# Optimization experiments

Hardware: AMD Instinct MI355X
Metric: run time of the kernel (lower is better)

The kernel has to match this reference:

```python
import jax, jax.numpy as jnp
import numpy as np

B, Cin, H, W = 8, 128, 64, 64
Cout, K, S, P = 128, 3, 1, 1
KK = K * K


def _conv(x, w, b=None):
    y = jax.lax.conv_general_dilated(
        x, w, window_strides=(S, S), padding=[(P, P), (P, P)],
        dimension_numbers=("NCHW", "OIHW", "NCHW"))
    if b is not None:
        y = y + b[None, :, None, None]
    return y


def setup_inputs() -> dict:
    key = jax.random.key(0)
    ks = jax.random.split(key, 6)
    x = jax.random.normal(ks[0], (B, Cin, H, W), jnp.float32)
    # offset/modulator convs are zero-init in the module; use small random
    # values so learned-offset sampling path is actually exercised.
    w_off = jax.random.normal(ks[1], (2 * KK, Cin, K, K), jnp.float32) * 0.01
    b_off = jax.random.normal(ks[2], (2 * KK,), jnp.float32) * 0.1
    w_mod = jax.random.normal(ks[3], (KK, Cin, K, K), jnp.float32) * 0.01
    b_mod = jax.random.normal(ks[4], (KK,), jnp.float32) * 0.1
    w_reg = jax.random.normal(ks[5], (Cout, Cin, K, K), jnp.float32) * (1.0 / np.sqrt(Cin * KK))
    return {"x": x, "w_off": w_off, "b_off": b_off,
            "w_mod": w_mod, "b_mod": b_mod, "w_reg": w_reg}


def _deform_conv2d(x, offset, mask, w_reg):
    # offset: [B, 2*KK, Hout, Wout] with (dy, dx) interleaved per tap (torchvision layout)
    Hout, Wout = offset.shape[2], offset.shape[3]
    off = offset.reshape(B, KK, 2, Hout, Wout)
    dy = off[:, :, 0].transpose(0, 2, 3, 1)  # [B,Hout,Wout,KK]
    dx = off[:, :, 1].transpose(0, 2, 3, 1)
    kh = (jnp.arange(KK) // K).astype(jnp.float32)
    kw = (jnp.arange(KK) % K).astype(jnp.float32)
    ho = jnp.arange(Hout, dtype=jnp.float32) * S - P
    wo = jnp.arange(Wout, dtype=jnp.float32) * S - P
    py = ho[None, :, None, None] + kh[None, None, None, :] + dy  # [B,Hout,Wout,KK]
    px = wo[None, None, :, None] + kw[None, None, None, :] + dx
    y0f = jnp.floor(py); x0f = jnp.floor(px)
    wy = (py - y0f)[..., None]; wx = (px - x0f)[..., None]
    y0 = y0f.astype(jnp.int32); x0 = x0f.astype(jnp.int32)
    x_bhwc = x.transpose(0, 2, 3, 1)  # [B,H,W,Cin]
    bidx = jnp.arange(B).reshape(B, 1, 1, 1)

    def gather(yi, xi):
        valid = ((yi >= 0) & (yi < H) & (xi >= 0) & (xi < W)).astype(x.dtype)
        v = x_bhwc[bidx, jnp.clip(yi, 0, H - 1), jnp.clip(xi, 0, W - 1)]
        return v * valid[..., None]  # [B,Hout,Wout,KK,Cin], zero outside

    v00 = gather(y0, x0)
    v01 = gather(y0, x0 + 1)
    v10 = gather(y0 + 1, x0)
    v11 = gather(y0 + 1, x0 + 1)
    val = (v00 * (1 - wy) * (1 - wx) + v01 * (1 - wy) * wx
           + v10 * wy * (1 - wx) + v11 * wy * wx)
    # modulated deformable conv v2: mask [B,KK,Hout,Wout]
    val = val * mask.transpose(0, 2, 3, 1)[..., None]
    # weighted accumulation over taps and input channels -> NCHW output
    return jnp.einsum("bhwkc,ock->bohw", val, w_reg.reshape(Cout, Cin, KK))


def reference(x, w_off, b_off, w_mod, b_mod, w_reg):
    offset = _conv(x, w_off, b_off)
    mask = 2.0 * jax.nn.sigmoid(_conv(x, w_mod, b_mod))
    return _deform_conv2d(x, offset, mask, w_reg)
```

## Files before the change

kernel.cpp:

```cpp
#include <hip/hip_runtime.h>
#include <hip/hip_bf16.h>
#include <math.h>

#define H 64
#define W 64
#define CIN 128
#define COUT 128
#define BATCH 8
#define NPIX (H*W)
#define PXT 32
#define AP  136
#define RP  36
#define VSZ (PXT*AP)

typedef __attribute__((ext_vector_type(8))) short bf16x8;
typedef __attribute__((ext_vector_type(2))) float f32x2;
typedef __attribute__((ext_vector_type(4))) float f32x4;
typedef __attribute__((ext_vector_type(16))) float f32x16;

static __device__ inline short f2bf(float f) {
  union { float f; unsigned u; } v; v.f = f;
  unsigned r = v.u + 0x7FFF + ((v.u >> 16) & 1);
  return (short)(r >> 16);
}
static __device__ inline f32x2 bfpair(unsigned u) {
  union { unsigned u; float f; } lo, hi;
  lo.u = u << 16; hi.u = u & 0xffff0000u;
  f32x2 r; r.x = lo.f; r.y = hi.f; return r;
}

__global__ __launch_bounds__(256) void k_prep(const float* __restrict__ x,
    short* __restrict__ xbh,
    const float* __restrict__ w_off, const float* __restrict__ w_mod,
    short* __restrict__ wOMs, const float* __restrict__ w_reg,
    short* __restrict__ wAs) {
  __shared__ float tile[32][65];
  int blk = blockIdx.x;
  int t = threadIdx.x;
  if (blk < 2048) {
    int cg = blk & 3, y = (blk >> 2) & 63, b = blk >> 8;
#pragma unroll
    for (int j = 0; j < 2; ++j) {
      int f = t + j * 256;
      int ci = f >> 4, xi4 = f & 15;
      float4 v = *(const float4*)&x[(((b * CIN + cg * 32 + ci) * H + y) * W) + xi4 * 4];
      *(float4*)&tile[ci][xi4 * 4] = v;
    }
    __syncthreads();
#pragma unroll
    for (int i = 0; i < 2; ++i) {
      int idx = t + i * 256;
      int xi = idx >> 3, cig = idx & 7;
      float f0 = tile[cig * 4 + 0][xi];
      float f1 = tile[cig * 4 + 1][xi];
      float f2 = tile[cig * 4 + 2][xi];
      float f3 = tile[cig * 4 + 3][xi];
      __hip_bfloat162 h01 = __float22bfloat162_rn(make_float2(f0, f1));
      __hip_bfloat162 h23 = __float22bfloat162_rn(make_float2(f2, f3));
      uint2 pk;
      pk.x = *(unsigned*)&h01; pk.y = *(unsigned*)&h23;
      *(uint2*)&xbh[((b * H + y) * W + xi) * CIN + cg * 32 + cig * 4] = pk;
    }
  } else if (blk < 2048 + 144) {
    int e = (blk - 2048) * 256 + t;
    int tap = e >> 12, oc = (e >> 7) & 31, c = e & 127;
    float v = 0.f;
    if (oc < 18)      v = w_off[(oc * 128 + c) * 9 + tap];
    else if (oc < 27) v = w_mod[((oc - 18) * 128 + c) * 9 + tap];
    int kstep = c >> 4, g = (c >> 3) & 1, j = c & 7;
    int lane = g * 32 + oc;
    int o = ((tap * 8 + kstep) * 64 + lane) * 8 + j;
    wOMs[o] = f2bf(v);
  } else {
    int e = (blk - 2192) * 256 + t;
    int tap = e >> 14, oc = (e >> 7) & 127, c = e & 127;
    int kstep = c >> 4, g = (c >> 3) & 1, j = c & 7;
    int ms = oc >> 5, m = oc & 31;
    int lane = g * 32 + m;
    int o = (((tap * 8 + kstep) * 4 + ms) * 64 + lane) * 8 + j;
    wAs[o] = f2bf(w_reg[(oc * 128 + c) * 9 + tap]);
  }
}

__global__ __launch_bounds__(512, 8) void k_deform(const short* __restrict__ xbh,
    const short* __restrict__ wOMs, const float* __restrict__ b_off,
    const float* __restrict__ b_mod, const short* __restrict__ wAs,
    float* __restrict__ out) {
  __shared__ __align__(16) char smem_u[31104];
  __shared__ __align__(16) float  pw[PXT * 9 * 4];
  __shared__ __align__(16) ushort pa4[PXT * 9 * 4];
  float* red  = (float*)smem_u;
  short* vs   = (short*)smem_u;
  float* redE = (float*)smem_u;

  int blk = blockIdx.x;
  int b = blk & 7, tile = blk >> 3;
  int pix0 = tile * PXT;
  int t = threadIdx.x;
  int lane = t & 63;
  int wv = t >> 6;
  int n32 = lane & 31, g = lane >> 5;

  const short* xbB = xbh + (size_t)b * NPIX * CIN;

  {
    f32x16 accO = {};
    int p0 = wv * 9;
    int tapA = p0 >> 3, tapB = (p0 + 8) >> 3;
    int gp = pix0 + n32;
    int yb = gp >> 6, xb = gp & 63;
    int yA = yb + tapA / 3 - 1, xA = xb + tapA % 3 - 1;
    int yB = yb + tapB / 3 - 1, xB = xb + tapB % 3 - 1;
    int okA = ((unsigned)yA < H) && ((unsigned)xA < W);
    int okB = ((unsigned)yB < H) && ((unsigned)xB < W);
    int linA = okA ? ((yA << 6) + xA) : 0;
    int linB = okB ? ((yB << 6) + xB) : 0;
#pragma unroll
    for (int u = 0; u < 9; ++u) {
      int pair = p0 + u;
      int kstep = pair & 7;
      int useB = (pair >> 3) != tapA;
      int lin = useB ? linB : linA;
      int ok  = useB ? okB  : okA;
      bf16x8 a = *(const bf16x8*)&wOMs[(pair * 64 + lane) * 8];
      int c0 = kstep * 16 + g * 8;
      bf16x8 bv = *(const bf16x8*)&xbB[(size_t)lin * CIN + c0];
      if (!ok) bv = (bf16x8){};
      accO = __builtin_amdgcn_mfma_f32_32x32x16_bf16(a, bv, accO, 0, 0, 0);
    }
#pragma unroll
    for (int r = 0; r < 16; ++r) {
      int row = (r & 3) + 8 * (r >> 2) + 4 * g;
      if (row < 27) red[wv * (27 * RP) + row * RP + n32] = accO[r];
    }
  }
  __syncthreads();

  for (int i = t; i < PXT * 9; i += 512) {
    int tap = i % 9, p = i / 9;
    float dyv = b_off[2 * tap], dxv = b_off[2 * tap + 1], z = b_mod[tap];
#pragma unroll
    for (int w = 0; w < 8; ++w) {
      const float* rw = red + w * (27 * RP);
      dyv += rw[(2 * tap) * RP + p];
      dxv += rw[(2 * tap + 1) * RP + p];
      z   += rw[(18 + tap) * RP + p];
    }
    float m = 2.f / (1.f + __expf(-z));
    int gp = pix0 + p;
    float py = (float)((gp >> 6) - 1 + tap / 3) + dyv;
    float pxx = (float)((gp & 63) - 1 + tap % 3) + dxv;
    float yf = floorf(py), xf = floorf(pxx);
    float wy = py - yf, wx = pxx - xf;
    int y0 = (int)yf, x0 = (int)xf;
    int y1 = y0 + 1, x1 = x0 + 1;
    float vy0 = ((unsigned)y0 < H) ? 1.f : 0.f;
    float vy1 = ((unsigned)y1 < H) ? 1.f : 0.f;
    float vx0 = ((unsigned)x0 < W) ? 1.f : 0.f;
    float vx1 = ((unsigned)x1 < W) ? 1.f : 0.f;
    int y0c = min(max(y0, 0), H - 1), y1c = min(max(y1, 0), H - 1);
    int x0c = min(max(x0, 0), W - 1), x1c = min(max(x1, 0), W - 1);
    *(float4*)&pw[i * 4] = make_float4((1.f - wy) * (1.f - wx) * m * vy0 * vx0,
                                       (1.f - wy) * wx * m * vy0 * vx1,
                                       wy * (1.f - wx) * m * vy1 * vx0,
                                       wy * wx * m * vy1 * vx1);
    pa4[i * 4 + 0] = (ushort)((y0c << 6) + x0c);
    pa4[i * 4 + 1] = (ushort)((y0c << 6) + x1c);
    pa4[i * 4 + 2] = (ushort)((y1c << 6) + x0c);
    pa4[i * 4 + 3] = (ushort)((y1c << 6) + x1c);
  }
  __syncthreads();

  int ms = wv & 3, ks = wv >> 2;
  int cq = t & 15, ps = t >> 4;
  int c0s = cq * 8;

  f32x16 acc = {};

  for (int tap = 0; tap < 9; ++tap) {
    short* vbuf = vs + (tap & 1) * VSZ;

    {
      int idx = (ps * 9 + tap) * 4;
      float4 wq = *(const float4*)&pw[idx];
      uint4 u00 = *(const uint4*)&xbB[(int)pa4[idx]     * CIN + c0s];
      uint4 u01 = *(const uint4*)&xbB[(int)pa4[idx + 1] * CIN + c0s];
      uint4 u10 = *(const uint4*)&xbB[(int)pa4[idx + 2] * CIN + c0s];
      uint4 u11 = *(const uint4*)&xbB[(int)pa4[idx + 3] * CIN + c0s];
      uint4 packed;
#pragma unroll
      for (int j = 0; j < 4; ++j) {
        f32x2 s = bfpair(((const unsigned*)&u00)[j]) * wq.x;
        s += bfpair(((const unsigned*)&u01)[j]) * wq.y;
        s += bfpair(((const unsigned*)&u10)[j]) * wq.z;
        s += bfpair(((const unsigned*)&u11)[j]) * wq.w;
        __hip_bfloat162 h2 = __float22bfloat162_rn(make_float2(s.x, s.y));
        ((unsigned*)&packed)[j] = *(unsigned*)&h2;
      }
      *(uint4*)&vbuf[ps * AP + c0s] = packed;
    }

    bf16x8 af[4];
#pragma unroll
    for (int i = 0; i < 4; ++i) {
      int kstep = ks * 4 + i;
      af[i] = *(const bf16x8*)&wAs[(((tap * 8 + kstep) * 4 + ms) * 64 + lane) * 8];
    }
    __syncthreads();

#pragma unroll
    for (int i = 0; i < 4; ++i) {
      int kstep = ks * 4 + i;
      int c0 = kstep * 16 + g * 8;
      bf16x8 bfr = *(const bf16x8*)&vbuf[n32 * AP + c0];
      acc = __builtin_amdgcn_mfma_f32_32x32x16_bf16(af[i], bfr, acc, 0, 0, 0);
    }
  }

  __syncthreads();
#pragma unroll
  for (int r = 0; r < 16; ++r) {
    if ((r < 8) == (ks == 1)) {
      int row = (r & 3) + 8 * (r >> 2) + 4 * g;
      redE[ms * (32 * 33) + row * 33 + n32] = acc[r];
    }
  }
  __syncthreads();
#pragma unroll
  for (int r = 0; r < 16; ++r) {
    if ((r < 8) == (ks == 0)) {
      int row = (r & 3) + 8 * (r >> 2) + 4 * g;
      float v = acc[r] + redE[ms * (32 * 33) + row * 33 + n32];
      out[(size_t)(b * COUT + ms * 32 + row) * NPIX + pix0 + n32] = v;
    }
  }
}

extern "C" void kernel_launch(void* const* d_in, const int* in_sizes, int n_in,
                              void* d_out, int out_size, void* d_ws, size_t ws_size,
                              hipStream_t stream) {
  const float* x     = (const float*)d_in[0];
  const float* w_off = (const float*)d_in[1];
  const float* b_off = (const float*)d_in[2];
  const float* w_mod = (const float*)d_in[3];
  const float* b_mod = (const float*)d_in[4];
  const float* w_reg = (const float*)d_in[5];

  short* xbh  = (short*)d_ws;
  short* wAs  = xbh + 4194304;
  short* wOMs = wAs + 147456;
  float* out  = (float*)d_out;

  k_prep<<<dim3(2768), 256, 0, stream>>>(x, xbh, w_off, w_mod, wOMs,
                                         w_reg, wAs);
  k_deform<<<dim3(NPIX / PXT * BATCH), 512, 0, stream>>>(
      xbh, wOMs, b_off, b_mod, wAs, out);
}
```

Measured before the change: 115.8 us.

## Process deform taps in pairs with quad-buffered LDS and restructure offset MFMA split

The main loop now samples two taps per iteration into four LDS buffers, so there are five barriers instead of nine and more gathers are in flight before each sync. The offset/mask conv is re-split so each wave handles one full tap plus one kstep of tap 8. The epilogue reduction is simplified so one k-half stores all rows and the other sums them. Launch bounds drop from 8 to 4 blocks per SM and LDS grows, which lowers occupancy. The sigmoid also switches from __expf to expf.

```diff
diff --git a/kernel.cpp b/kernel.cpp
--- a/kernel.cpp
+++ b/kernel.cpp
@@ -82,11 +82,11 @@
   }
 }
 
-__global__ __launch_bounds__(512, 8) void k_deform(const short* __restrict__ xbh,
+__global__ __launch_bounds__(512, 4) void k_deform(const short* __restrict__ xbh,
     const short* __restrict__ wOMs, const float* __restrict__ b_off,
     const float* __restrict__ b_mod, const short* __restrict__ wAs,
     float* __restrict__ out) {
-  __shared__ __align__(16) char smem_u[31104];
+  __shared__ __align__(16) char smem_u[34816];
   __shared__ __align__(16) float  pw[PXT * 9 * 4];
   __shared__ __align__(16) ushort pa4[PXT * 9 * 4];
   float* red  = (float*)smem_u;
@@ -105,25 +105,27 @@
 
   {
     f32x16 accO = {};
-    int p0 = wv * 9;
-    int tapA = p0 >> 3, tapB = (p0 + 8) >> 3;
     int gp = pix0 + n32;
     int yb = gp >> 6, xb = gp & 63;
-    int yA = yb + tapA / 3 - 1, xA = xb + tapA % 3 - 1;
-    int yB = yb + tapB / 3 - 1, xB = xb + tapB % 3 - 1;
-    int okA = ((unsigned)yA < H) && ((unsigned)xA < W);
-    int okB = ((unsigned)yB < H) && ((unsigned)xB < W);
-    int linA = okA ? ((yA << 6) + xA) : 0;
-    int linB = okB ? ((yB << 6) + xB) : 0;
-#pragma unroll
-    for (int u = 0; u < 9; ++u) {
-      int pair = p0 + u;
-      int kstep = pair & 7;
-      int useB = (pair >> 3) != tapA;
-      int lin = useB ? linB : linA;
-      int ok  = useB ? okB  : okA;
-      bf16x8 a = *(const bf16x8*)&wOMs[(pair * 64 + lane) * 8];
-      int c0 = kstep * 16 + g * 8;
+    {
+      int y = yb + wv / 3 - 1, x = xb + wv % 3 - 1;
+      int ok = ((unsigned)y < H) && ((unsigned)x < W);
+      int lin = ok ? ((y << 6) + x) : 0;
+#pragma unroll
+      for (int kstep = 0; kstep < 8; ++kstep) {
+        bf16x8 a = *(const bf16x8*)&wOMs[((wv * 8 + kstep) * 64 + lane) * 8];
+        int c0 = kstep * 16 + g * 8;
+        bf16x8 bv = *(const bf16x8*)&xbB[(size_t)lin * CIN + c0];
+        if (!ok) bv = (bf16x8){};
+        accO = __builtin_amdgcn_mfma_f32_32x32x16_bf16(a, bv, accO, 0, 0, 0);
+      }
+    }
+    {
+      int y = yb + 1, x = xb + 1;
+      int ok = (y < H) && (x < W);
+      int lin = ok ? ((y << 6) + x) : 0;
+      bf16x8 a = *(const bf16x8*)&wOMs[((8 * 8 + wv) * 64 + lane) * 8];
+      int c0 = wv * 16 + g * 8;
       bf16x8 bv = *(const bf16x8*)&xbB[(size_t)lin * CIN + c0];
       if (!ok) bv = (bf16x8){};
       accO = __builtin_amdgcn_mfma_f32_32x32x16_bf16(a, bv, accO, 0, 0, 0);
@@ -146,7 +148,7 @@
       dxv += rw[(2 * tap + 1) * RP + p];
       z   += rw[(18 + tap) * RP + p];
     }
-    float m = 2.f / (1.f + __expf(-z));
+    float m = 2.f / (1.f + expf(-z));
     int gp = pix0 + p;
     float py = (float)((gp >> 6) - 1 + tap / 3) + dyv;
     float pxx = (float)((gp & 63) - 1 + tap % 3) + dxv;
@@ -177,34 +179,42 @@
 
   f32x16 acc = {};
 
-  for (int tap = 0; tap < 9; ++tap) {
-    short* vbuf = vs + (tap & 1) * VSZ;
-
-    {
-      int idx = (ps * 9 + tap) * 4;
-      float4 wq = *(const float4*)&pw[idx];
-      uint4 u00 = *(const uint4*)&xbB[(int)pa4[idx]     * CIN + c0s];
-      uint4 u01 = *(const uint4*)&xbB[(int)pa4[idx + 1] * CIN + c0s];
-      uint4 u10 = *(const uint4*)&xbB[(int)pa4[idx + 2] * CIN + c0s];
-      uint4 u11 = *(const uint4*)&xbB[(int)pa4[idx + 3] * CIN + c0s];
-      uint4 packed;
-#pragma unroll
-      for (int j = 0; j < 4; ++j) {
-        f32x2 s = bfpair(((const unsigned*)&u00)[j]) * wq.x;
-        s += bfpair(((const unsigned*)&u01)[j]) * wq.y;
-        s += bfpair(((const unsigned*)&u10)[j]) * wq.z;
-        s += bfpair(((const unsigned*)&u11)[j]) * wq.w;
-        __hip_bfloat162 h2 = __float22bfloat162_rn(make_float2(s.x, s.y));
-        ((unsigned*)&packed)[j] = *(unsigned*)&h2;
-      }
-      *(uint4*)&vbuf[ps * AP + c0s] = packed;
-    }
-
-    bf16x8 af[4];
+  auto sample = [&](int tap, short* vbuf) {
+    int idx = (ps * 9 + tap) * 4;
+    float4 wq = *(const float4*)&pw[idx];
+    uint4 u00 = *(const uint4*)&xbB[(int)pa4[idx]     * CIN + c0s];
+    uint4 u01 = *(const uint4*)&xbB[(int)pa4[idx + 1] * CIN + c0s];
+    uint4 u10 = *(const uint4*)&xbB[(int)pa4[idx + 2] * CIN + c0s];
+    uint4 u11 = *(const uint4*)&xbB[(int)pa4[idx + 3] * CIN + c0s];
+    uint4 packed;
+#pragma unroll
+    for (int j = 0; j < 4; ++j) {
+      f32x2 s = bfpair(((const unsigned*)&u00)[j]) * wq.x;
+      s += bfpair(((const unsigned*)&u01)[j]) * wq.y;
+      s += bfpair(((const unsigned*)&u10)[j]) * wq.z;
+      s += bfpair(((const unsigned*)&u11)[j]) * wq.w;
+      __hip_bfloat162 h2 = __float22bfloat162_rn(make_float2(s.x, s.y));
+      ((unsigned*)&packed)[j] = *(unsigned*)&h2;
+    }
+    *(uint4*)&vbuf[ps * AP + c0s] = packed;
+  };
+
+#pragma unroll
+  for (int pi = 0; pi < 5; ++pi) {
+    int tp = pi * 2;
+    short* vb0 = vs + ((pi & 1) * 2) * VSZ;
+    short* vb1 = vb0 + VSZ;
+
+    sample(tp, vb0);
+    if (tp + 1 < 9) sample(tp + 1, vb1);
+
+    bf16x8 af0[4], af1[4];
 #pragma unroll
     for (int i = 0; i < 4; ++i) {
       int kstep = ks * 4 + i;
-      af[i] = *(const bf16x8*)&wAs[(((tap * 8 + kstep) * 4 + ms) * 64 + lane) * 8];
+      af0[i] = *(const bf16x8*)&wAs[(((tp * 8 + kstep) * 4 + ms) * 64 + lane) * 8];
+      if (tp + 1 < 9)
+        af1[i] = *(const bf16x8*)&wAs[((((tp + 1) * 8 + kstep) * 4 + ms) * 64 + lane) * 8];
     }
     __syncthreads();
 
@@ -212,23 +222,32 @@
     for (int i = 0; i < 4; ++i) {
       int kstep = ks * 4 + i;
       int c0 = kstep * 16 + g * 8;
-      bf16x8 bfr = *(const bf16x8*)&vbuf[n32 * AP + c0];
-      acc = __builtin_amdgcn_mfma_f32_32x32x16_bf16(af[i], bfr, acc, 0, 0, 0);
-    }
-  }
-
-  __syncthreads();
-#pragma unroll
-  for (int r = 0; r < 16; ++r) {
-    if ((r < 8) == (ks == 1)) {
+      bf16x8 bfr = *(const bf16x8*)&vb0[n32 * AP + c0];
+      acc = __builtin_amdgcn_mfma_f32_32x32x16_bf16(af0[i], bfr, acc, 0, 0, 0);
+    }
+    if (tp + 1 < 9) {
+#pragma unroll
+      for (int i = 0; i < 4; ++i) {
+        int kstep = ks * 4 + i;
+        int c0 = kstep * 16 + g * 8;
+        bf16x8 bfr = *(const bf16x8*)&vb1[n32 * AP + c0];
+        acc = __builtin_amdgcn_mfma_f32_32x32x16_bf16(af1[i], bfr, acc, 0, 0, 0);
+      }
+    }
+  }
+
+  __syncthreads();
+  if (ks == 1) {
+#pragma unroll
+    for (int r = 0; r < 16; ++r) {
       int row = (r & 3) + 8 * (r >> 2) + 4 * g;
       redE[ms * (32 * 33) + row * 33 + n32] = acc[r];
     }
   }
   __syncthreads();
-#pragma unroll
-  for (int r = 0; r < 16; ++r) {
-    if ((r < 8) == (ks == 0)) {
+  if (ks == 0) {
+#pragma unroll
+    for (int r = 0; r < 16; ++r) {
       int row = (r & 3) + 8 * (r >> 2) + 4 * g;
       float v = acc[r] + redE[ms * (32 * 33) + row * 33 + n32];
       out[(size_t)(b * COUT + ms * 32 + row) * NPIX + pix0 + n32] = v;
```

After: 110.4 us. 1.05x faster.

## Double pixel tile per block and restructure offset conv by tap per wave

Applied to the files above, without the earlier changes.

Each block now handles a full 64-pixel row instead of 32 pixels. The offset/mask conv is reorganised so each wave owns one tap and reuses its weight fragment across two pixel halves, with the ninth tap split across waves. The main MFMA loop also reuses the A fragments for two B tiles, and the final reduction is done in two halves. This halves the number of blocks and the weight reloads per pixel, at the cost of doubled LDS, lower occupancy (launch bounds 4), and fewer blocks to spread across CUs.

```diff
diff --git a/kernel.cpp b/kernel.cpp
--- a/kernel.cpp
+++ b/kernel.cpp
@@ -8,9 +8,9 @@
 #define COUT 128
 #define BATCH 8
 #define NPIX (H*W)
-#define PXT 32
+#define PXT 64
 #define AP  136
-#define RP  36
+#define RP  68
 #define VSZ (PXT*AP)
 
 typedef __attribute__((ext_vector_type(8))) short bf16x8;
@@ -82,11 +82,11 @@
   }
 }
 
-__global__ __launch_bounds__(512, 8) void k_deform(const short* __restrict__ xbh,
+__global__ __launch_bounds__(512, 4) void k_deform(const short* __restrict__ xbh,
     const short* __restrict__ wOMs, const float* __restrict__ b_off,
     const float* __restrict__ b_mod, const short* __restrict__ wAs,
     float* __restrict__ out) {
-  __shared__ __align__(16) char smem_u[31104];
+  __shared__ __align__(16) char smem_u[58752];
   __shared__ __align__(16) float  pw[PXT * 9 * 4];
   __shared__ __align__(16) ushort pa4[PXT * 9 * 4];
   float* red  = (float*)smem_u;
@@ -104,34 +104,50 @@
   const short* xbB = xbh + (size_t)b * NPIX * CIN;
 
   {
-    f32x16 accO = {};
-    int p0 = wv * 9;
-    int tapA = p0 >> 3, tapB = (p0 + 8) >> 3;
-    int gp = pix0 + n32;
-    int yb = gp >> 6, xb = gp & 63;
-    int yA = yb + tapA / 3 - 1, xA = xb + tapA % 3 - 1;
-    int yB = yb + tapB / 3 - 1, xB = xb + tapB % 3 - 1;
-    int okA = ((unsigned)yA < H) && ((unsigned)xA < W);
-    int okB = ((unsigned)yB < H) && ((unsigned)xB < W);
-    int linA = okA ? ((yA << 6) + xA) : 0;
-    int linB = okB ? ((yB << 6) + xB) : 0;
-#pragma unroll
-    for (int u = 0; u < 9; ++u) {
-      int pair = p0 + u;
-      int kstep = pair & 7;
-      int useB = (pair >> 3) != tapA;
-      int lin = useB ? linB : linA;
-      int ok  = useB ? okB  : okA;
-      bf16x8 a = *(const bf16x8*)&wOMs[(pair * 64 + lane) * 8];
+    f32x16 accO0 = {}, accO1 = {};
+    int dy = wv / 3 - 1, dx = wv % 3 - 1;
+    int y = tile + dy;
+    int okY = ((unsigned)y < H);
+    int xA = n32 + dx, xB = 32 + n32 + dx;
+    int ok0 = okY && ((unsigned)xA < W);
+    int ok1 = okY && ((unsigned)xB < W);
+    int lin0 = ok0 ? ((y << 6) + xA) : 0;
+    int lin1 = ok1 ? ((y << 6) + xB) : 0;
+#pragma unroll
+    for (int kstep = 0; kstep < 8; ++kstep) {
+      bf16x8 a = *(const bf16x8*)&wOMs[((wv * 8 + kstep) * 64 + lane) * 8];
       int c0 = kstep * 16 + g * 8;
-      bf16x8 bv = *(const bf16x8*)&xbB[(size_t)lin * CIN + c0];
-      if (!ok) bv = (bf16x8){};
-      accO = __builtin_amdgcn_mfma_f32_32x32x16_bf16(a, bv, accO, 0, 0, 0);
+      bf16x8 bv0 = *(const bf16x8*)&xbB[(size_t)lin0 * CIN + c0];
+      if (!ok0) bv0 = (bf16x8){};
+      accO0 = __builtin_amdgcn_mfma_f32_32x32x16_bf16(a, bv0, accO0, 0, 0, 0);
+      bf16x8 bv1 = *(const bf16x8*)&xbB[(size_t)lin1 * CIN + c0];
+      if (!ok1) bv1 = (bf16x8){};
+      accO1 = __builtin_amdgcn_mfma_f32_32x32x16_bf16(a, bv1, accO1, 0, 0, 0);
+    }
+    {
+      int y8 = tile + 1;
+      int okY8 = (y8 < H);
+      int x8A = n32 + 1, x8B = 32 + n32 + 1;
+      int ok80 = okY8 && (x8A < W);
+      int ok81 = okY8 && (x8B < W);
+      int l80 = ok80 ? ((y8 << 6) + x8A) : 0;
+      int l81 = ok81 ? ((y8 << 6) + x8B) : 0;
+      bf16x8 a8 = *(const bf16x8*)&wOMs[((8 * 8 + wv) * 64 + lane) * 8];
+      int c0 = wv * 16 + g * 8;
+      bf16x8 bv0 = *(const bf16x8*)&xbB[(size_t)l80 * CIN + c0];
+      if (!ok80) bv0 = (bf16x8){};
+      accO0 = __builtin_amdgcn_mfma_f32_32x32x16_bf16(a8, bv0, accO0, 0, 0, 0);
+      bf16x8 bv1 = *(const bf16x8*)&xbB[(size_t)l81 * CIN + c0];
+      if (!ok81) bv1 = (bf16x8){};
+      accO1 = __builtin_amdgcn_mfma_f32_32x32x16_bf16(a8, bv1, accO1, 0, 0, 0);
     }
 #pragma unroll
     for (int r = 0; r < 16; ++r) {
       int row = (r & 3) + 8 * (r >> 2) + 4 * g;
-      if (row < 27) red[wv * (27 * RP) + row * RP + n32] = accO[r];
+      if (row < 27) {
+        red[wv * (27 * RP) + row * RP + n32]      = accO0[r];
+        red[wv * (27 * RP) + row * RP + 32 + n32] = accO1[r];
+      }
     }
   }
   __syncthreads();
@@ -146,7 +162,7 @@
       dxv += rw[(2 * tap + 1) * RP + p];
       z   += rw[(18 + tap) * RP + p];
     }
-    float m = 2.f / (1.f + __expf(-z));
+    float m = 2.f / (1.f + expf(-z));
     int gp = pix0 + p;
     float py = (float)((gp >> 6) - 1 + tap / 3) + dyv;
     float pxx = (float)((gp & 63) - 1 + tap % 3) + dxv;
@@ -175,30 +191,34 @@
   int cq = t & 15, ps = t >> 4;
   int c0s = cq * 8;
 
-  f32x16 acc = {};
+  f32x16 acc0 = {}, acc1 = {};
+
+  auto sampleOne = [&](int px, int tap, short* vbuf) {
+    int idx = (px * 9 + tap) * 4;
+    uint2 pk = *(const uint2*)&pa4[idx];
+    float4 wq = *(const float4*)&pw[idx];
+    uint4 u00 = *(const uint4*)&xbB[(int)(pk.x & 0xffffu) * CIN + c0s];
+    uint4 u01 = *(const uint4*)&xbB[(int)(pk.x >> 16)     * CIN + c0s];
+    uint4 u10 = *(const uint4*)&xbB[(int)(pk.y & 0xffffu) * CIN + c0s];
+    uint4 u11 = *(const uint4*)&xbB[(int)(pk.y >> 16)     * CIN + c0s];
+    uint4 packed;
+#pragma unroll
+    for (int j = 0; j < 4; ++j) {
+      f32x2 s = bfpair(((const unsigned*)&u00)[j]) * wq.x;
+      s += bfpair(((const unsigned*)&u01)[j]) * wq.y;
+      s += bfpair(((const unsigned*)&u10)[j]) * wq.z;
+      s += bfpair(((const unsigned*)&u11)[j]) * wq.w;
+      __hip_bfloat162 h2 = __float22bfloat162_rn(make_float2(s.x, s.y));
+      ((unsigned*)&packed)[j] = *(unsigned*)&h2;
+    }
+    *(uint4*)&vbuf[px * AP + c0s] = packed;
+  };
 
   for (int tap = 0; tap < 9; ++tap) {
     short* vbuf = vs + (tap & 1) * VSZ;
 
-    {
-      int idx = (ps * 9 + tap) * 4;
-      float4 wq = *(const float4*)&pw[idx];
-      uint4 u00 = *(const uint4*)&xbB[(int)pa4[idx]     * CIN + c0s];
-      uint4 u01 = *(const uint4*)&xbB[(int)pa4[idx + 1] * CIN + c0s];
-      uint4 u10 = *(const uint4*)&xbB[(int)pa4[idx + 2] * CIN + c0s];
-      uint4 u11 = *(const uint4*)&xbB[(int)pa4[idx + 3] * CIN + c0s];
-      uint4 packed;
-#pragma unroll
-      for (int j = 0; j < 4; ++j) {
-        f32x2 s = bfpair(((const unsigned*)&u00)[j]) * wq.x;
-        s += bfpair(((const unsigned*)&u01)[j]) * wq.y;
-        s += bfpair(((const unsigned*)&u10)[j]) * wq.z;
-        s += bfpair(((const unsigned*)&u11)[j]) * wq.w;
-        __hip_bfloat162 h2 = __float22bfloat162_rn(make_float2(s.x, s.y));
-        ((unsigned*)&packed)[j] = *(unsigned*)&h2;
-      }
-      *(uint4*)&vbuf[ps * AP + c0s] = packed;
-    }
+    sampleOne(ps, tap, vbuf);
+    sampleOne(ps + 32, tap, vbuf);
 
     bf16x8 af[4];
 #pragma unroll
@@ -211,27 +231,34 @@
 #pragma unroll
     for (int i = 0; i < 4; ++i) {
       int kstep = ks * 4 + i;
-      int c0 = kstep * 16 + g * 8;
-      bf16x8 bfr = *(const bf16x8*)&vbuf[n32 * AP + c0];
-      acc = __builtin_amdgcn_mfma_f32_32x32x16_bf16(af[i], bfr, acc, 0, 0, 0);
-    }
-  }
-
-  __syncthreads();
-#pragma unroll
-  for (int r = 0; r < 16; ++r) {
-    if ((r < 8) == (ks == 1)) {
-      int row = (r & 3) + 8 * (r >> 2) + 4 * g;
-      redE[ms * (32 * 33) + row * 33 + n32] = acc[r];
-    }
-  }
-  __syncthreads();
-#pragma unroll
-  for (int r = 0; r < 16; ++r) {
-    if ((r < 8) == (ks == 0)) {
-      int row = (r & 3) + 8 * (r >> 2) + 4 * g;
-      float v = acc[r] + redE[ms * (32 * 33) + row * 33 + n32];
-      out[(size_t)(b * COUT + ms * 32 + row) * NPIX + pix0 + n32] = v;
+      int c0r = kstep * 16 + g * 8;
+      bf16x8 b0 = *(const bf16x8*)&vbuf[n32 * AP + c0r];
+      acc0 = __builtin_amdgcn_mfma_f32_32x32x16_bf16(af[i], b0, acc0, 0, 0, 0);
+      bf16x8 b1 = *(const bf16x8*)&vbuf[(32 + n32) * AP + c0r];
+      acc1 = __builtin_amdgcn_mfma_f32_32x32x16_bf16(af[i], b1, acc1, 0, 0, 0);
+    }
+  }
+
+#pragma unroll
+  for (int h = 0; h < 2; ++h) {
+    __syncthreads();
+    if (ks == 1) {
+#pragma unroll
+      for (int r = 0; r < 16; ++r) {
+        int row = (r & 3) + 8 * (r >> 2) + 4 * g;
+        float v = (h == 0) ? acc0[r] : acc1[r];
+        redE[ms * (32 * 33) + row * 33 + n32] = v;
+      }
+    }
+    __syncthreads();
+    if (ks == 0) {
+#pragma unroll
+      for (int r = 0; r < 16; ++r) {
+        int row = (r & 3) + 8 * (r >> 2) + 4 * g;
+        float v = ((h == 0) ? acc0[r] : acc1[r])
+                + redE[ms * (32 * 33) + row * 33 + n32];
+        out[(size_t)(b * COUT + ms * 32 + row) * NPIX + pix0 + h * 32 + n32] = v;
+      }
     }
   }
 }
```

After: 110.3 us. 4.7% less time.
